# Performance work log

Measured on AMD Instinct MI355X. Metric: run time of the kernel, lower is better.

## Reference

```python
import jax, jax.numpy as jnp
import numpy as np

TOP_K = 2


def setup_inputs() -> dict:
    key = jax.random.key(0)
    ks = jax.random.split(key, 10)
    B, S, H, E = 4, 2048, 1024, 8
    s = 1.0 / np.sqrt(H)
    x = jax.random.normal(ks[0], (B, S, H), dtype=jnp.float32)
    gate_w = jax.random.normal(ks[1], (H, E), dtype=jnp.float32) * s
    gate_b = jnp.zeros((E,), dtype=jnp.float32)
    w1 = jax.random.normal(ks[2], (E, H, H), dtype=jnp.float32) * s
    b1 = jnp.zeros((E, H), dtype=jnp.float32)
    w2 = jax.random.normal(ks[3], (E, H, H), dtype=jnp.float32) * s
    b2 = jnp.zeros((E, H), dtype=jnp.float32)
    w3 = jax.random.normal(ks[4], (E, H, H), dtype=jnp.float32) * s
    b3 = jnp.zeros((E, H), dtype=jnp.float32)
    return {"x": x, "gate_w": gate_w, "gate_b": gate_b,
            "w1": w1, "b1": b1, "w2": w2, "b2": b2, "w3": w3, "b3": b3}


def reference(x, gate_w, gate_b, w1, b1, w2, b2, w3, b3):
    B, S, H = x.shape
    t = x.reshape(-1, H)                                  # [T, H]
    T = t.shape[0]
    # Router: logits -> fp32 softmax -> top-k -> renormalize
    router_logits = t @ gate_w + gate_b                   # [T, E]
    probs = jax.nn.softmax(router_logits.astype(jnp.float32), axis=-1)
    w, idx = jax.lax.top_k(probs, TOP_K)                  # [T, K]
    w = w / jnp.sum(w, axis=-1, keepdims=True)
    w = w.astype(x.dtype)
    # Dense combine weights: cw[t, e] = router weight if expert e selected for token t, else 0
    rows = jnp.arange(T)[:, None]
    cw = jnp.zeros(router_logits.shape, dtype=x.dtype).at[rows, idx].add(w)  # [T, E]
    # Expert MLPs (relu(fc1) -> relu(fc2) -> fc3), batched over experts
    h1 = jax.nn.relu(jnp.einsum('th,ehf->etf', t, w1) + b1[:, None, :])
    h2 = jax.nn.relu(jnp.einsum('etf,efg->etg', h1, w2) + b2[:, None, :])
    y = jnp.einsum('etg,egh->eth', h2, w3) + b3[:, None, :]                 # [E, T, H]
    # Weighted combine (equivalent to per-expert gather + weighted index_add)
    out = jnp.einsum('te,eth->th', cw, y)                 # [T, H]
    return out.reshape(B, S, H), router_logits
```

## Files before the change

### kernel.cpp

```cpp
#include <hip/hip_runtime.h>
#include <hip/hip_bf16.h>


#define HDIM 1024
#define NEXP 8
#define BM 128
#define BN 128
#define BK 32
#define HH ((size_t)HDIM * HDIM)

typedef __hip_bfloat16 bf16;
typedef unsigned short ushort_t;
typedef __attribute__((ext_vector_type(8))) short bf16x8;
typedef __attribute__((ext_vector_type(4))) float f32x4;

__device__ __forceinline__ float bflo(unsigned u) { return __uint_as_float(u << 16); }
__device__ __forceinline__ float bfhi(unsigned u) { return __uint_as_float(u & 0xffff0000u); }
__device__ __forceinline__ unsigned short f2bfu(float f) {
  bf16 h = __float2bfloat16(f);
  return *reinterpret_cast<unsigned short*>(&h);
}
__device__ __forceinline__ int iclamp(int v, int lo, int hi) {
  return v < lo ? lo : (v > hi ? hi : v);
}

__device__ __forceinline__ void async_cp16(const void* g, void* l) {
  __builtin_amdgcn_global_load_lds((const __attribute__((address_space(1))) void*)g,
                                   (__attribute__((address_space(3))) void*)l,
                                   16, 0, 0);
}

__device__ __forceinline__ void ld4f(const void* base, size_t idx, bool f32, float o[4]) {
  if (f32) {
    float4 v = *(const float4*)((const float*)base + idx);
    o[0] = v.x; o[1] = v.y; o[2] = v.z; o[3] = v.w;
  } else {
    uint2 v = *(const uint2*)((const unsigned short*)base + idx);
    o[0] = bflo(v.x); o[1] = bfhi(v.x); o[2] = bflo(v.y); o[3] = bfhi(v.y);
  }
}

__global__ void k_init(int* __restrict__ meta) {
  int i = blockIdx.x * blockDim.x + threadIdx.x;
  if (i < 3072) meta[i] = 0;
}

__global__ void k_sniff(const ushort_t* a0, int n0, const ushort_t* a1, int n1,
                        const ushort_t* a2, int n2, const ushort_t* a3, int n3,
                        const ushort_t* a4, int n4, int* __restrict__ flags) {
  int b = blockIdx.x;
  const ushort_t* a = b == 0 ? a0 : b == 1 ? a1 : b == 2 ? a2 : b == 3 ? a3 : a4;
  int n = b == 0 ? n0 : b == 1 ? n1 : b == 2 ? n2 : b == 3 ? n3 : n4;
  int hits = 0;
  for (int i = threadIdx.x; i < n; i += 256) {
    ushort_t v = a[i];
    if ((v & 0x7F80) == 0x7F80) hits++;
  }
  if (hits) atomicAdd(&flags[b], hits);
}

__global__ __launch_bounds__(512) void k_router(
    const void* __restrict__ x, const void* __restrict__ gw,
    const bf16* __restrict__ gb, void* __restrict__ dout, bf16* __restrict__ xb,
    int* __restrict__ sel_e, float* __restrict__ sel_w,
    int* __restrict__ meta, int TS, int T) {
  __shared__ float sgT[NEXP][HDIM];
  const int* flags = meta + 2048;
  bool fx = flags[0] != 0, fgw = flags[1] != 0;
  int tid = threadIdx.x;

#pragma unroll
  for (int r = 0; r < 2; r++) {
    int h = r * 512 + tid;
    float g[8];
    ld4f(gw, (size_t)h * NEXP, fgw, g);
    ld4f(gw, (size_t)h * NEXP + 4, fgw, g + 4);
#pragma unroll
    for (int e = 0; e < NEXP; e++) sgT[e][h] = g[e];
  }
  __syncthreads();

  int wave = tid >> 6, lane = tid & 63;
  int t = blockIdx.x * 8 + wave;

  double acc[NEXP];
#pragma unroll
  for (int e = 0; e < NEXP; e++) acc[e] = 0.0;

  if (t < T) {
#pragma unroll
    for (int j = 0; j < 4; j++) {
      int h = j * 256 + lane * 4;
      float xf[4];
      ld4f(x, (size_t)t * HDIM + h, fx, xf);
      if (fx) {
        uint2 ov;
        ov.x = (unsigned)f2bfu(xf[0]) | ((unsigned)f2bfu(xf[1]) << 16);
        ov.y = (unsigned)f2bfu(xf[2]) | ((unsigned)f2bfu(xf[3]) << 16);
        *(uint2*)((unsigned short*)xb + (size_t)t * HDIM + h) = ov;
      }
#pragma unroll
      for (int e = 0; e < NEXP; e++) {
        float4 g = *(const float4*)&sgT[e][h];
        acc[e] += (double)xf[0] * (double)g.x + (double)xf[1] * (double)g.y
                + (double)xf[2] * (double)g.z + (double)xf[3] * (double)g.w;
      }
    }
  }

#pragma unroll
  for (int off = 32; off >= 1; off >>= 1) {
#pragma unroll
    for (int e = 0; e < NEXP; e++) acc[e] += __shfl_down(acc[e], off);
  }

  if (lane == 0 && t < T) {
    double l[NEXP];
#pragma unroll
    for (int e = 0; e < NEXP; e++) l[e] = acc[e] + (double)__bfloat162float(gb[e]);
    size_t lo = (size_t)T * HDIM + (size_t)t * NEXP;
    if (fx) {
      float* lp = (float*)dout + lo;
#pragma unroll
      for (int e = 0; e < NEXP; e++) lp[e] = (float)l[e];
    } else {
      unsigned short* lp = (unsigned short*)dout + lo;
#pragma unroll
      for (int e = 0; e < NEXP; e++) lp[e] = f2bfu((float)l[e]);
    }
    int i1 = 0; double v1 = l[0];
#pragma unroll
    for (int e = 1; e < NEXP; e++) if (l[e] > v1) { v1 = l[e]; i1 = e; }
    int i2 = -1; double v2 = -1e300;
#pragma unroll
    for (int e = 0; e < NEXP; e++) if (e != i1 && l[e] > v2) { v2 = l[e]; i2 = e; }
    if (i2 < 0) i2 = (i1 + 1) & 7;
    float w1 = 1.0f / (1.0f + __expf((float)(v2 - v1)));
    sel_e[2 * t] = i1; sel_e[2 * t + 1] = i2;
    sel_w[2 * t] = w1; sel_w[2 * t + 1] = 1.0f - w1;
  }
}

__global__ void k_offsets(const int* __restrict__ sel_e, int* __restrict__ meta,
                          int* __restrict__ list, int* __restrict__ row_e,
                          int RCAP, int NTMAX, int TS) {
  int s = blockIdx.x;
  __shared__ int base[NEXP + 1];
  __shared__ int wsum[4][NEXP];
  int tid = threadIdx.x;

  int cnt[NEXP];
#pragma unroll
  for (int e = 0; e < NEXP; e++) cnt[e] = 0;
  const int* se = sel_e + (size_t)2 * s * TS;
  for (int i = tid; i < 2 * TS; i += 256) {
    int v = se[i];
#pragma unroll
    for (int e = 0; e < NEXP; e++) cnt[e] += (v == e) ? 1 : 0;
  }
#pragma unroll
  for (int off = 32; off >= 1; off >>= 1)
#pragma unroll
    for (int e = 0; e < NEXP; e++) cnt[e] += __shfl_down(cnt[e], off);
  int lane = tid & 63, wave = tid >> 6;
  if (lane == 0) {
#pragma unroll
    for (int e = 0; e < NEXP; e++) wsum[wave][e] = cnt[e];
  }
  __syncthreads();

  if (tid == 0) {
    int b = 0;
    for (int e = 0; e < NEXP; e++) {
      int ce = wsum[0][e] + wsum[1][e] + wsum[2][e] + wsum[3][e];
      base[e] = b;
      meta[s * 8 + e] = ce;
      meta[512 + s * 8 + e] = b;
      meta[1024 + s * 8 + e] = b;
      b = (b + ce + BM - 1) & ~(BM - 1);
    }
    base[NEXP] = b;
    meta[2560 + s] = b / BM;
  }
  __syncthreads();

  for (int r = tid; r < NTMAX; r += blockDim.x) {
    int rs = r * BM;
    int e = 0;
    for (int q = 1; q < NEXP; q++) if (rs >= base[q]) e = q;
    row_e[s * NTMAX + r] = e;
  }
  int* ls = list + (size_t)s * RCAP;
  for (int e = 0; e < NEXP; e++) {
    int ce = wsum[0][e] + wsum[1][e] + wsum[2][e] + wsum[3][e];
    for (int p = base[e] + ce + tid; p < base[e + 1]; p += blockDim.x)
      ls[p] = s * TS;
  }
}

__global__ void k_scatter(const int* __restrict__ sel_e, int* __restrict__ meta,
                          int* __restrict__ list, int* __restrict__ pos_of,
                          int T, int TS, int RCAP) {
  int t = blockIdx.x * blockDim.x + threadIdx.x;
  if (t >= T) return;
  int s = t / TS;
#pragma unroll
  for (int k = 0; k < 2; k++) {
    int e = sel_e[2 * t + k];
    int pos = atomicAdd(&meta[512 + s * 8 + e], 1);
    if (pos >= 0 && pos < RCAP) list[(size_t)s * RCAP + pos] = t;
    pos_of[2 * t + k] = pos;
  }
}

__global__ void k_trans(const void* __restrict__ w, const int* __restrict__ flags,
                        int fidx, bf16* __restrict__ wt) {
  int e = blockIdx.z;
  bool fW = flags[fidx] != 0;
  __shared__ unsigned short tile[32][33];
  int tid = threadIdx.x;
  int r = tid >> 3, c4 = (tid & 7) * 4;
  int R0 = blockIdx.y * 32, C0 = blockIdx.x * 32;
  float v[4];
  ld4f(w, (size_t)e * HH + (size_t)(R0 + r) * HDIM + C0 + c4, fW, v);
  tile[c4 + 0][r] = f2bfu(v[0]);
  tile[c4 + 1][r] = f2bfu(v[1]);
  tile[c4 + 2][r] = f2bfu(v[2]);
  tile[c4 + 3][r] = f2bfu(v[3]);
  __syncthreads();
  uint2 ov;
  ov.x = (unsigned)tile[r][c4 + 0] | ((unsigned)tile[r][c4 + 1] << 16);
  ov.y = (unsigned)tile[r][c4 + 2] | ((unsigned)tile[r][c4 + 3] << 16);
  *(uint2*)((unsigned short*)wt + (size_t)e * HH + (size_t)(C0 + r) * HDIM + R0 + c4) = ov;
}

template <bool GATHER, bool RELU>
__global__ __launch_bounds__(256) void k_gemm(
    const bf16* __restrict__ A, const bf16* __restrict__ Axb,
    const int* __restrict__ list,
    const int* __restrict__ row_e, const int* __restrict__ ntiles,
    const bf16* __restrict__ wt, const bf16* __restrict__ bias,
    bf16* __restrict__ C, const int* __restrict__ flags, int Tm1) {
  int id = blockIdx.y * gridDim.x + blockIdx.x;
  int tm = id % gridDim.y;
  int tn = id / gridDim.y;
  if (tm >= *ntiles) return;
  int e = row_e[tm];
  int row0 = tm * BM;
  const bf16* Ause = (GATHER && flags[0] != 0) ? Axb : A;

  __shared__ __align__(16) unsigned short lA[3 * BM * BK];
  __shared__ __align__(16) unsigned short lB[3 * BN * BK];

  int tid = threadIdx.x;
  int lane = tid & 63, wave = tid >> 6;
  int ksw = ((lane & 3) ^ ((lane >> 3) & 3)) * 8;
  int r0 = wave * 32 + (lane >> 2);

  const unsigned short* pb0 = (const unsigned short*)wt + (size_t)e * HH
                            + (size_t)(tn * BN + r0) * HDIM + ksw;
  const unsigned short* pb1 = pb0 + (size_t)16 * HDIM;
  const unsigned short* pa0;
  const unsigned short* pa1;
  if (GATHER) {
    int t0 = iclamp(list[row0 + r0], 0, Tm1);
    int t1 = iclamp(list[row0 + r0 + 16], 0, Tm1);
    pa0 = (const unsigned short*)Ause + (size_t)t0 * HDIM + ksw;
    pa1 = (const unsigned short*)Ause + (size_t)t1 * HDIM + ksw;
  } else {
    pa0 = (const unsigned short*)Ause + (size_t)(row0 + r0) * HDIM + ksw;
    pa1 = pa0 + (size_t)16 * HDIM;
  }
  unsigned short* laD0 = lA + (wave * 32) * BK;
  unsigned short* laD1 = laD0 + 16 * BK;
  unsigned short* lbD0 = lB + (wave * 32) * BK;
  unsigned short* lbD1 = lbD0 + 16 * BK;

#define STAGE(pb, ktt)                                         \
  do {                                                         \
    int _o = (pb) * (BM * BK);                                 \
    async_cp16(pa0 + (size_t)(ktt) * BK, laD0 + _o);           \
    async_cp16(pa1 + (size_t)(ktt) * BK, laD1 + _o);           \
    async_cp16(pb0 + (size_t)(ktt) * BK, lbD0 + _o);           \
    async_cp16(pb1 + (size_t)(ktt) * BK, lbD1 + _o);           \
  } while (0)

  f32x4 acc[4][4];
#pragma unroll
  for (int i = 0; i < 4; i++)
#pragma unroll
    for (int j = 0; j < 4; j++) acc[i][j] = (f32x4){0.f, 0.f, 0.f, 0.f};

  int lm = lane & 15, quad = lane >> 4;
  int am = (wave & 1) * 64, bn = (wave >> 1) * 64;
  int rdc = (quad ^ ((lm >> 1) & 3)) * 8;

  STAGE(0, 0);
  STAGE(1, 1);
  STAGE(2, 2);

  const int NK = HDIM / BK;
  int p = 0;
  for (int kt = 0; kt < NK; ++kt) {
    if (kt < NK - 2)       asm volatile("s_waitcnt vmcnt(8)" ::: "memory");
    else if (kt == NK - 2) asm volatile("s_waitcnt vmcnt(4)" ::: "memory");
    else                   asm volatile("s_waitcnt vmcnt(0)" ::: "memory");
    __builtin_amdgcn_sched_barrier(0);
    __builtin_amdgcn_s_barrier();
    __builtin_amdgcn_sched_barrier(0);

    int o = p * (BM * BK);
    bf16x8 af[4], bfr[4];
#pragma unroll
    for (int i = 0; i < 4; i++)
      af[i] = *(const bf16x8*)&lA[o + (am + i * 16 + lm) * BK + rdc];
#pragma unroll
    for (int j = 0; j < 4; j++)
      bfr[j] = *(const bf16x8*)&lB[o + (bn + j * 16 + lm) * BK + rdc];
    __builtin_amdgcn_s_setprio(1);
#pragma unroll
    for (int i = 0; i < 4; i++)
#pragma unroll
      for (int j = 0; j < 4; j++)
        acc[i][j] = __builtin_amdgcn_mfma_f32_16x16x32_bf16(af[i], bfr[j], acc[i][j], 0, 0, 0);
    __builtin_amdgcn_s_setprio(0);

    __builtin_amdgcn_sched_barrier(0);
    __builtin_amdgcn_s_barrier();
    __builtin_amdgcn_sched_barrier(0);
    if (kt + 3 < NK) STAGE(p, kt + 3);
    p = (p == 2) ? 0 : p + 1;
  }
#undef STAGE

#pragma unroll
  for (int j = 0; j < 4; j++) {
    int col = tn * BN + bn + j * 16 + lm;
    float bv = __bfloat162float(bias[e * HDIM + col]);
#pragma unroll
    for (int i = 0; i < 4; i++) {
      int rowb = row0 + am + i * 16 + quad * 4;
#pragma unroll
      for (int rr = 0; rr < 4; rr++) {
        float v = acc[i][j][rr] + bv;
        if (RELU) v = fmaxf(v, 0.f);
        ((unsigned short*)C)[(size_t)(rowb + rr) * HDIM + col] = f2bfu(v);
      }
    }
  }
}

__global__ void k_combine(const bf16* __restrict__ y, const int* __restrict__ pos_of,
                          const float* __restrict__ sel_w, void* __restrict__ dout,
                          size_t out_elem_off, const int* __restrict__ meta, int Pm1) {
  bool fx = meta[2048] != 0;
  int t = blockIdx.x;
  int tid = threadIdx.x;
  int p0 = iclamp(pos_of[2 * t], 0, Pm1);
  int p1 = iclamp(pos_of[2 * t + 1], 0, Pm1);
  float w0 = sel_w[2 * t], w1 = sel_w[2 * t + 1];
  int h = tid * 4;
  uint2 a = *(const uint2*)((const unsigned short*)y + (size_t)p0 * HDIM + h);
  uint2 b = *(const uint2*)((const unsigned short*)y + (size_t)p1 * HDIM + h);
  float o0 = w0 * bflo(a.x) + w1 * bflo(b.x);
  float o1 = w0 * bfhi(a.x) + w1 * bfhi(b.x);
  float o2 = w0 * bflo(a.y) + w1 * bflo(b.y);
  float o3 = w0 * bfhi(a.y) + w1 * bfhi(b.y);
  size_t off = out_elem_off + (size_t)t * HDIM + h;
  if (fx) {
    float4 ov = { o0, o1, o2, o3 };
    *(float4*)((float*)dout + off) = ov;
  } else {
    uint2 ov;
    ov.x = (unsigned)f2bfu(o0) | ((unsigned)f2bfu(o1) << 16);
    ov.y = (unsigned)f2bfu(o2) | ((unsigned)f2bfu(o3) << 16);
    *(uint2*)((unsigned short*)dout + off) = ov;
  }
}

extern "C" void kernel_launch(void* const* d_in, const int* in_sizes, int n_in,
                              void* d_out, int out_size, void* d_ws, size_t ws_size,
                              hipStream_t stream) {
  const void* x  = d_in[0];
  const void* gw = d_in[1];
  const bf16* gb = (const bf16*)d_in[2];
  const void* w1 = d_in[3];
  const bf16* b1 = (const bf16*)d_in[4];
  const void* w2 = d_in[5];
  const bf16* b2 = (const bf16*)d_in[6];
  const void* w3 = d_in[7];
  const bf16* b3 = (const bf16*)d_in[8];

  const int T = in_sizes[0] / HDIM;
  const size_t wtsz = (size_t)NEXP * HH * 2;
  const size_t xbsz = (size_t)T * HDIM * 2;

  int S = 64;
  size_t base_need = 0;
  for (int cand = 1; cand <= 64; cand *= 2) {
    size_t rcap = (size_t)2 * T / cand + NEXP * BM;
    size_t ntmx = rcap / BM;
    size_t need = 12288 + (size_t)8 * T * 3 + (size_t)4 * cand * rcap
                + (size_t)4 * cand * ntmx + wtsz + 2 * rcap * HDIM * 2
                + xbsz + 1024;
    if (need <= ws_size) { S = cand; base_need = need; break; }
  }
  const int TS = T / S;
  const int RCAP = 2 * TS + NEXP * BM;
  const int NTMAX = RCAP / BM;
  const bool hoist = (S > 1) && (base_need + 2 * wtsz <= ws_size);

  char* ws = (char*)d_ws;
  size_t ofs = 0;
  int*   meta   = (int*)(ws + ofs);   ofs += 12288;
  int*   sel_e  = (int*)(ws + ofs);   ofs += (size_t)8 * T;
  float* sel_w  = (float*)(ws + ofs); ofs += (size_t)8 * T;
  int*   pos_of = (int*)(ws + ofs);   ofs += (size_t)8 * T;
  int*   list   = (int*)(ws + ofs);   ofs += (size_t)4 * S * RCAP;
  int*   row_e  = (int*)(ws + ofs);   ofs += (size_t)4 * S * NTMAX;
  ofs = (ofs + 255) & ~(size_t)255;
  bf16* wt0 = (bf16*)(ws + ofs); ofs += wtsz;
  bf16* h1  = (bf16*)(ws + ofs); ofs += (size_t)RCAP * HDIM * 2;
  bf16* h2  = (bf16*)(ws + ofs); ofs += (size_t)RCAP * HDIM * 2;
  bf16* xb  = (bf16*)(ws + ofs); ofs += xbsz;
  bf16* wt1 = wt0;
  bf16* wt2 = wt0;
  if (hoist) {
    wt1 = (bf16*)(ws + ofs); ofs += wtsz;
    wt2 = (bf16*)(ws + ofs); ofs += wtsz;
  }

  int* flags = meta + 2048;

  k_init<<<12, 256, 0, stream>>>(meta);
  k_sniff<<<5, 256, 0, stream>>>((const ushort_t*)x, 32768,
                                 (const ushort_t*)gw, HDIM * NEXP,
                                 (const ushort_t*)w1, 32768,
                                 (const ushort_t*)w2, 32768,
                                 (const ushort_t*)w3, 32768, flags);
  k_router<<<(T + 7) / 8, 512, 0, stream>>>(x, gw, gb, d_out, xb, sel_e, sel_w,
                                            meta, TS, T);
  k_offsets<<<S, 256, 0, stream>>>(sel_e, meta, list, row_e, RCAP, NTMAX, TS);
  k_scatter<<<(T + 255) / 256, 256, 0, stream>>>(sel_e, meta, list, pos_of, T, TS, RCAP);

  dim3 tg(HDIM / 32, HDIM / 32, NEXP);
  dim3 gg(HDIM / BN, NTMAX);
  const bf16* xbf = (const bf16*)x;

  if (hoist) {
    k_trans<<<tg, 256, 0, stream>>>(w1, flags, 2, wt0);
    k_trans<<<tg, 256, 0, stream>>>(w2, flags, 3, wt1);
    k_trans<<<tg, 256, 0, stream>>>(w3, flags, 4, wt2);
  }
  for (int s = 0; s < S; s++) {
    const int* lst = list + (size_t)s * RCAP;
    const int* re  = row_e + (size_t)s * NTMAX;
    const int* nt  = meta + 2560 + s;
    if (!hoist) k_trans<<<tg, 256, 0, stream>>>(w1, flags, 2, wt0);
    k_gemm<true,  true ><<<gg, 256, 0, stream>>>(xbf, xb, lst, re, nt, wt0, b1, h1, flags, T - 1);
    if (!hoist) k_trans<<<tg, 256, 0, stream>>>(w2, flags, 3, wt1);
    k_gemm<false, true ><<<gg, 256, 0, stream>>>(h1, nullptr, nullptr, re, nt, wt1, b2, h2, flags, T - 1);
    if (!hoist) k_trans<<<tg, 256, 0, stream>>>(w3, flags, 4, wt2);
    k_gemm<false, false><<<gg, 256, 0, stream>>>(h2, nullptr, nullptr, re, nt, wt2, b3, h1, flags, T - 1);
    k_combine<<<TS, 256, 0, stream>>>(h1, pos_of + (size_t)2 * s * TS,
                                      sel_w + (size_t)2 * s * TS,
                                      d_out, (size_t)s * TS * HDIM, meta, RCAP - 1);
  }
}
```

Baseline: 487.2 us.

## Use double-buffered GEMM pipeline and block-aggregated atomics in scatter

The expert GEMM's LDS pipeline drops from triple buffering (prefetch depth 3) to double buffering (depth 2). This halves shared-memory use per block, which may allow more resident blocks, but leaves less latency hiding per block. The scatter kernel now counts per-expert slots in shared memory and issues one global atomic per expert per block instead of one per token-expert pair. The launch sizes blocks to divide the segment length, which assumes T is divisible by the block size and that blocks never cross segments.

```diff
diff --git a/kernel.cpp b/kernel.cpp
--- a/kernel.cpp
+++ b/kernel.cpp
@@ -201,16 +201,25 @@
 __global__ void k_scatter(const int* __restrict__ sel_e, int* __restrict__ meta,
                           int* __restrict__ list, int* __restrict__ pos_of,
                           int T, int TS, int RCAP) {
-  int t = blockIdx.x * blockDim.x + threadIdx.x;
-  if (t >= T) return;
-  int s = t / TS;
-#pragma unroll
-  for (int k = 0; k < 2; k++) {
-    int e = sel_e[2 * t + k];
-    int pos = atomicAdd(&meta[512 + s * 8 + e], 1);
-    if (pos >= 0 && pos < RCAP) list[(size_t)s * RCAP + pos] = t;
-    pos_of[2 * t + k] = pos;
-  }
+  __shared__ int lcnt[NEXP];
+  __shared__ int lbase[NEXP];
+  int tid = threadIdx.x;
+  if (tid < NEXP) lcnt[tid] = 0;
+  __syncthreads();
+  int t = blockIdx.x * blockDim.x + tid;
+  int s = (int)(((long long)blockIdx.x * blockDim.x) / TS);
+  int e0 = sel_e[2 * t], e1 = sel_e[2 * t + 1];
+  int r0 = atomicAdd(&lcnt[e0], 1);
+  int r1 = atomicAdd(&lcnt[e1], 1);
+  __syncthreads();
+  if (tid < NEXP) lbase[tid] = atomicAdd(&meta[512 + s * 8 + tid], lcnt[tid]);
+  __syncthreads();
+  int p0 = lbase[e0] + r0;
+  int p1 = lbase[e1] + r1;
+  if (p0 >= 0 && p0 < RCAP) list[(size_t)s * RCAP + p0] = t;
+  if (p1 >= 0 && p1 < RCAP) list[(size_t)s * RCAP + p1] = t;
+  pos_of[2 * t] = p0;
+  pos_of[2 * t + 1] = p1;
 }
 
 __global__ void k_trans(const void* __restrict__ w, const int* __restrict__ flags,
@@ -249,8 +258,8 @@
   int row0 = tm * BM;
   const bf16* Ause = (GATHER && flags[0] != 0) ? Axb : A;
 
-  __shared__ __align__(16) unsigned short lA[3 * BM * BK];
-  __shared__ __align__(16) unsigned short lB[3 * BN * BK];
+  __shared__ __align__(16) unsigned short lA[2 * BM * BK];
+  __shared__ __align__(16) unsigned short lB[2 * BN * BK];
 
   int tid = threadIdx.x;
   int lane = tid & 63, wave = tid >> 6;
@@ -297,14 +306,12 @@
 
   STAGE(0, 0);
   STAGE(1, 1);
-  STAGE(2, 2);
 
   const int NK = HDIM / BK;
-  int p = 0;
   for (int kt = 0; kt < NK; ++kt) {
-    if (kt < NK - 2)       asm volatile("s_waitcnt vmcnt(8)" ::: "memory");
-    else if (kt == NK - 2) asm volatile("s_waitcnt vmcnt(4)" ::: "memory");
-    else                   asm volatile("s_waitcnt vmcnt(0)" ::: "memory");
+    int p = kt & 1;
+    if (kt < NK - 1) asm volatile("s_waitcnt vmcnt(4)" ::: "memory");
+    else             asm volatile("s_waitcnt vmcnt(0)" ::: "memory");
     __builtin_amdgcn_sched_barrier(0);
     __builtin_amdgcn_s_barrier();
     __builtin_amdgcn_sched_barrier(0);
@@ -328,8 +335,7 @@
     __builtin_amdgcn_sched_barrier(0);
     __builtin_amdgcn_s_barrier();
     __builtin_amdgcn_sched_barrier(0);
-    if (kt + 3 < NK) STAGE(p, kt + 3);
-    p = (p == 2) ? 0 : p + 1;
+    if (kt + 2 < NK) STAGE(p, kt + 2);
   }
 #undef STAGE
 
@@ -441,7 +447,10 @@
   k_router<<<(T + 7) / 8, 512, 0, stream>>>(x, gw, gb, d_out, xb, sel_e, sel_w,
                                             meta, TS, T);
   k_offsets<<<S, 256, 0, stream>>>(sel_e, meta, list, row_e, RCAP, NTMAX, TS);
-  k_scatter<<<(T + 255) / 256, 256, 0, stream>>>(sel_e, meta, list, pos_of, T, TS, RCAP);
+  {
+    int sbd = TS < 256 ? TS : 256;
+    k_scatter<<<T / sbd, sbd, 0, stream>>>(sel_e, meta, list, pos_of, T, TS, RCAP);
+  }
 
   dim3 tg(HDIM / 32, HDIM / 32, NEXP);
   dim3 gg(HDIM / BN, NTMAX);
```

New measurement: 432.9 us. 11.1% less time.
